# Performance work log

Hardware: AMD Instinct MI355X
Metric: run time of the kernel (lower is better)

The kernel has to match this reference:

```python
import jax, jax.numpy as jnp
import numpy as np

B, A, HR = 2, 180, 512
H_OUT = W_OUT = 512


def setup_inputs() -> dict:
    key = jax.random.key(0)
    k1, = jax.random.split(key, 1)
    sino = jax.random.normal(k1, (B, A, HR), dtype=jnp.float32)
    angles_deg = jnp.linspace(0.0, 180.0, A, endpoint=False, dtype=jnp.float32)
    return {"sino": sino, "angles_deg": angles_deg, "H": H_OUT, "W": W_OUT}


def _forward(sino, angles_deg, H, W):
    Bn, An, Hr = sino.shape
    pad = int(1.0 * 0.1 * min(H, W))  # pad_ratio = 1.0
    Hp, Wp = H + 2 * pad, W + 2 * pad

    # --- F.interpolate bilinear, align_corners=False: (A,B,Hr,1) -> (A,B,Hp,Wp).
    # Input width is 1, so width interp replicates the single column; only height interp matters.
    src = jnp.clip((jnp.arange(Hp, dtype=jnp.float32) + 0.5) * (Hr / Hp) - 0.5, 0.0, Hr - 1)
    i0 = jnp.floor(src).astype(jnp.int32)
    i1 = jnp.minimum(i0 + 1, Hr - 1)
    wH = src - i0.astype(jnp.float32)
    p = jnp.transpose(sino, (1, 0, 2)).astype(jnp.float32)  # (A,B,Hr)
    col = p[:, :, i0] * (1.0 - wH) + p[:, :, i1] * wH       # (A,B,Hp)
    proj = jnp.broadcast_to(col[:, :, :, None], (An, Bn, Hp, Wp))  # (A,B,Hp,Wp)

    # --- affine_grid (align_corners=False), sign = -1
    th = -jnp.deg2rad(angles_deg)
    c, s = jnp.cos(th), jnp.sin(th)                          # (A,)
    xs = (jnp.arange(Wp, dtype=jnp.float32) + 0.5) * (2.0 / Wp) - 1.0
    ys = (jnp.arange(Hp, dtype=jnp.float32) + 0.5) * (2.0 / Hp) - 1.0
    gx = c[:, None, None] * xs[None, None, :] - s[:, None, None] * ys[None, :, None]  # (A,Hp,Wp)
    gy = s[:, None, None] * xs[None, None, :] + c[:, None, None] * ys[None, :, None]

    # --- grid_sample bilinear, zeros padding, align_corners=False
    ix = ((gx + 1.0) * Wp - 1.0) * 0.5
    iy = ((gy + 1.0) * Hp - 1.0) * 0.5
    x0 = jnp.floor(ix).astype(jnp.int32); x1 = x0 + 1
    y0 = jnp.floor(iy).astype(jnp.int32); y1 = y0 + 1
    wx = ix - x0.astype(jnp.float32)
    wy = iy - y0.astype(jnp.float32)

    def corner(img, xi, yi, w):  # img (B,Hp,Wp); idx/w (Hp,Wp)
        valid = (xi >= 0) & (xi <= Wp - 1) & (yi >= 0) & (yi <= Hp - 1)
        xc = jnp.clip(xi, 0, Wp - 1)
        yc = jnp.clip(yi, 0, Hp - 1)
        return img[:, yc, xc] * (w * valid.astype(jnp.float32))[None]

    def sample(img, x0a, x1a, y0a, y1a, wxa, wya):
        return (corner(img, x0a, y0a, (1 - wxa) * (1 - wya)) +
                corner(img, x1a, y0a, wxa * (1 - wya)) +
                corner(img, x0a, y1a, (1 - wxa) * wya) +
                corner(img, x1a, y1a, wxa * wya))

    xr = jax.vmap(sample)(proj, x0, x1, y0, y1, wx, wy)      # (A,B,Hp,Wp)
    acc = xr.sum(axis=0) / (An + 1e-06)                      # (B,Hp,Wp)
    acc = acc[:, None, :, :]                                 # (B,1,Hp,Wp)
    if pad > 0:
        acc = acc[:, :, pad:Hp - pad, pad:Wp - pad]
    return acc


def reference(sino, angles_deg, H, W):
    return _forward(sino, angles_deg, H, W)
```

## Files before the change

### kernel.cpp

```cpp
#include <hip/hip_runtime.h>
#include <hip/hip_fp16.h>
#include <math.h>

#define B_N   2
#define A_N   180
#define HR_N  512
#define H_OUT 512
#define W_OUT 512
#define PAD   51
#define HP    614
#define WP    614
#define GUARD 80
#define HPP   (HP + 2*GUARD)
#define NPIX  (H_OUT * W_OUT)

#define TW     16
#define TH     8
#define HALF_A 90
#define CH     30
#define NCH    (HALF_A / CH)
#define WIN    20


__device__ __forceinline__ float col_val(const float* __restrict__ sino,
                                         int b, int a, int yy) {
    if (yy < 0 || yy >= HP) return 0.0f;
    float src = ((float)yy + 0.5f) * ((float)HR_N / (float)HP) - 0.5f;
    src = fminf(fmaxf(src, 0.0f), (float)(HR_N - 1));
    int i0 = (int)floorf(src);
    int i1 = min(i0 + 1, HR_N - 1);
    float wH = src - (float)i0;
    const float* srow = sino + ((size_t)b * A_N + a) * HR_N;
    return srow[i0] * (1.0f - wH) + srow[i1] * wH;
}

__global__ void prep_kernel(const float* __restrict__ sino,
                            const float* __restrict__ angles,
                            uint2* __restrict__ pk2,
                            float2* __restrict__ tg) {
    int idx = blockIdx.x * blockDim.x + threadIdx.x;
    if (idx < A_N) {
        float th = -angles[idx] * (float)(M_PI / 180.0);
        tg[idx] = make_float2(cosf(th), sinf(th));
    }
    const int total = A_N * HPP;
    if (idx < total) {
        int y = idx % HPP;
        int a = idx / HPP;
        int yy = y - GUARD;
        float v00 = col_val(sino, 0, a, yy);
        float v10 = col_val(sino, 1, a, yy);
        float v01 = col_val(sino, 0, a, yy + 1);
        float v11 = col_val(sino, 1, a, yy + 1);
        __half2 lo = __floats2half2_rn(v00, v10);
        __half2 hi = __floats2half2_rn(v01, v11);
        uint2 u;
        u.x = *(unsigned int*)&lo;
        u.y = *(unsigned int*)&hi;
        pk2[idx] = u;
    }
}

__global__ __launch_bounds__(256, 8) void bp_kernel(const uint2* __restrict__ pk2,
                                                    const float2* __restrict__ tgv,
                                                    float* __restrict__ out) {
    __shared__ int   s_base[A_N];
    __shared__ uint2 s_win[2 * CH * WIN];
    __shared__ float s_red[2][128];

    int t  = threadIdx.x;
    int tx = blockIdx.x, ty = blockIdx.y;
    float Xc = (float)(tx * TW) - 248.0f;
    float Yc = (float)(ty * TH) - 252.0f;

    if (t < A_N) {
        float2 cs = tgv[t];
        float iyc = fmaf(cs.y, Xc, fmaf(cs.x, Yc, 306.5f));
        s_base[t] = (int)floorf(iyc) - 9;
    }

    int half = t >> 7;
    int tt   = t & 127;
    int lx = tt & (TW - 1), ly = tt >> 4;
    float X = (float)(tx * TW + lx) - 255.5f;
    float Y = (float)(ty * TH + ly) - 255.5f;

    float acc0 = 0.0f, acc1 = 0.0f;
    __syncthreads();

    bool interior = (Xc * Xc + Yc * Yc) <= 87500.0f;

    for (int ch = 0; ch < NCH; ++ch) {
        for (int e = t; e < 2 * CH * WIN; e += 256) {
            int hh = e / (CH * WIN);
            int r  = e - hh * (CH * WIN);
            int la = r / WIN;
            int j  = r - la * WIN;
            int a  = hh * HALF_A + ch * CH + la;
            s_win[e] = pk2[(size_t)a * HPP + (GUARD + s_base[a] + j)];
        }
        __syncthreads();

        const int aoff = half * HALF_A + ch * CH;
        const int woff = half * (CH * WIN);
        if (interior) {
            __half2 hacc = __float2half2_rn(0.0f);
#pragma unroll
            for (int la = 0; la < CH; ++la) {
                float2 cs = tgv[aoff + la];
                float c = cs.x, s = cs.y;
                float iyc = fmaf(s, Xc, fmaf(c, Yc, 306.5f));
                float Kf  = 315.5f - floorf(iyc);
                float f   = fmaf(s, X, fmaf(c, Y, Kf));
                int   li  = (int)f;
                float wy  = f - (float)li;
                uint2 cv  = s_win[woff + la * WIN + li];
                __half2 lo = *(__half2*)&cv.x;
                __half2 hi = *(__half2*)&cv.y;
                __half2 r2 = __hfma2(__float2half2_rn(wy), __hsub2(hi, lo), lo);
                hacc = __hadd2(hacc, r2);
            }
            acc0 += __low2float(hacc);
            acc1 += __high2float(hacc);
        } else {
#pragma unroll
            for (int la = 0; la < CH; ++la) {
                float2 cs = tgv[aoff + la];
                float c = cs.x, s = cs.y;
                float iyc = fmaf(s, Xc, fmaf(c, Yc, 306.5f));
                float Kf  = 315.5f - floorf(iyc);
                float f   = fmaf(s, X, fmaf(c, Y, Kf));
                int   li  = (int)f;
                float wy  = f - (float)li;
                uint2 cv  = s_win[woff + la * WIN + li];
                __half2 lo = *(__half2*)&cv.x;
                __half2 hi = *(__half2*)&cv.y;
                __half2 r2 = __hfma2(__float2half2_rn(wy), __hsub2(hi, lo), lo);
                float ix = fmaf(c, X, fmaf(-s, Y, 306.5f));
                float xf = fminf(fmaxf(ix + 1.0f, 0.0f), 1.0f)
                         * fminf(fmaxf((float)WP - ix, 0.0f), 1.0f);
                acc0 = fmaf(xf, __low2float(r2), acc0);
                acc1 = fmaf(xf, __high2float(r2), acc1);
            }
        }
        __syncthreads();
    }

    if (half) {
        s_red[0][tt] = acc0;
        s_red[1][tt] = acc1;
    }
    __syncthreads();
    if (!half) {
        const float inv = 1.0f / (180.0f + 1e-6f);
        float a0 = (acc0 + s_red[0][tt]) * inv;
        float a1 = (acc1 + s_red[1][tt]) * inv;
        int idx = (ty * TH + ly) * W_OUT + (tx * TW + lx);
        out[idx]        = a0;
        out[NPIX + idx] = a1;
    }
}

extern "C" void kernel_launch(void* const* d_in, const int* in_sizes, int n_in,
                              void* d_out, int out_size, void* d_ws, size_t ws_size,
                              hipStream_t stream) {
    const float* sino   = (const float*)d_in[0];
    const float* angles = (const float*)d_in[1];
    char*   ws  = (char*)d_ws;
    uint2*  pk2 = (uint2*)ws;
    float2* tg  = (float2*)(ws + (size_t)A_N * HPP * sizeof(uint2));

    const int total = A_N * HPP;
    prep_kernel<<<(total + 255) / 256, 256, 0, stream>>>(sino, angles, pk2, tg);

    dim3 grid(W_OUT / TW, H_OUT / TH);
    bp_kernel<<<grid, 256, 0, stream>>>(pk2, tg, (float*)d_out);
}
```

Measured before the change: 86.66 us.

## Split angles four ways with two pixels per thread and cached trig in LDS

```diff
diff --git a/kernel.cpp b/kernel.cpp
--- a/kernel.cpp
+++ b/kernel.cpp
@@ -14,12 +14,12 @@
 #define HPP   (HP + 2*GUARD)
 #define NPIX  (H_OUT * W_OUT)
 
-#define TW     16
-#define TH     8
-#define HALF_A 90
-#define CH     30
-#define NCH    (HALF_A / CH)
-#define WIN    20
+#define TW    16
+#define TH    8
+#define QA    45
+#define CH_Q  15
+#define NCH   3
+#define WIN   20
 
 
 __device__ __forceinline__ float col_val(const float* __restrict__ sino,
@@ -61,12 +61,89 @@
     }
 }
 
+template <bool INTERIOR>
+__device__ __forceinline__ void bp_body(const uint2* __restrict__ pk2,
+                                        const float2* __restrict__ s_tg,
+                                        const int* __restrict__ s_base,
+                                        uint2* __restrict__ s_win,
+                                        int t, int q, float X, float Y,
+                                        float Xc, float Yc,
+                                        float& a00, float& a01, float& a10, float& a11) {
+    for (int ch = 0; ch < NCH; ++ch) {
+        for (int e = t; e < 4 * CH_Q * WIN; e += 256) {
+            int wid = e / WIN;
+            int j   = e - wid * WIN;
+            int qq  = wid / CH_Q;
+            int la  = wid - qq * CH_Q;
+            int a   = qq * QA + ch * CH_Q + la;
+            s_win[e] = pk2[(size_t)a * HPP + (GUARD + s_base[a] + j)];
+        }
+        __syncthreads();
+
+        const int abase = q * QA + ch * CH_Q;
+        const int wbase = q * (CH_Q * WIN);
+        if (INTERIOR) {
+            __half2 h0 = __float2half2_rn(0.0f);
+            __half2 h1 = __float2half2_rn(0.0f);
+#pragma unroll
+            for (int la = 0; la < CH_Q; ++la) {
+                float2 cs = s_tg[abase + la];
+                float c = cs.x, s = cs.y;
+                float iyc = fmaf(s, Xc, fmaf(c, Yc, 306.5f));
+                float Kf  = 315.5f - floorf(iyc);
+                float f0  = fmaf(s, X, fmaf(c, Y, Kf));
+                float f1  = f0 + s;
+                int   li0 = (int)f0;  float wy0 = f0 - (float)li0;
+                int   li1 = (int)f1;  float wy1 = f1 - (float)li1;
+                uint2 cv0 = s_win[wbase + la * WIN + li0];
+                uint2 cv1 = s_win[wbase + la * WIN + li1];
+                __half2 lo0 = *(__half2*)&cv0.x, hi0 = *(__half2*)&cv0.y;
+                __half2 lo1 = *(__half2*)&cv1.x, hi1 = *(__half2*)&cv1.y;
+                h0 = __hadd2(h0, __hfma2(__float2half2_rn(wy0), __hsub2(hi0, lo0), lo0));
+                h1 = __hadd2(h1, __hfma2(__float2half2_rn(wy1), __hsub2(hi1, lo1), lo1));
+            }
+            a00 += __low2float(h0);  a01 += __high2float(h0);
+            a10 += __low2float(h1);  a11 += __high2float(h1);
+        } else {
+#pragma unroll
+            for (int la = 0; la < CH_Q; ++la) {
+                float2 cs = s_tg[abase + la];
+                float c = cs.x, s = cs.y;
+                float iyc = fmaf(s, Xc, fmaf(c, Yc, 306.5f));
+                float Kf  = 315.5f - floorf(iyc);
+                float f0  = fmaf(s, X, fmaf(c, Y, Kf));
+                float f1  = f0 + s;
+                int   li0 = (int)f0;  float wy0 = f0 - (float)li0;
+                int   li1 = (int)f1;  float wy1 = f1 - (float)li1;
+                uint2 cv0 = s_win[wbase + la * WIN + li0];
+                uint2 cv1 = s_win[wbase + la * WIN + li1];
+                __half2 lo0 = *(__half2*)&cv0.x, hi0 = *(__half2*)&cv0.y;
+                __half2 lo1 = *(__half2*)&cv1.x, hi1 = *(__half2*)&cv1.y;
+                __half2 r0 = __hfma2(__float2half2_rn(wy0), __hsub2(hi0, lo0), lo0);
+                __half2 r1 = __hfma2(__float2half2_rn(wy1), __hsub2(hi1, lo1), lo1);
+                float ix0 = fmaf(c, X, fmaf(-s, Y, 306.5f));
+                float ix1 = ix0 + c;
+                float xf0 = fminf(fmaxf(ix0 + 1.0f, 0.0f), 1.0f)
+                          * fminf(fmaxf((float)WP - ix0, 0.0f), 1.0f);
+                float xf1 = fminf(fmaxf(ix1 + 1.0f, 0.0f), 1.0f)
+                          * fminf(fmaxf((float)WP - ix1, 0.0f), 1.0f);
+                a00 = fmaf(xf0, __low2float(r0),  a00);
+                a01 = fmaf(xf0, __high2float(r0), a01);
+                a10 = fmaf(xf1, __low2float(r1),  a10);
+                a11 = fmaf(xf1, __high2float(r1), a11);
+            }
+        }
+        __syncthreads();
+    }
+}
+
 __global__ __launch_bounds__(256, 8) void bp_kernel(const uint2* __restrict__ pk2,
                                                     const float2* __restrict__ tgv,
                                                     float* __restrict__ out) {
-    __shared__ int   s_base[A_N];
-    __shared__ uint2 s_win[2 * CH * WIN];
-    __shared__ float s_red[2][128];
+    __shared__ float2 s_tg[A_N];
+    __shared__ int    s_base[A_N];
+    __shared__ uint2  s_win[4 * CH_Q * WIN];
+    __shared__ float  s_red[3][256];
 
     int t  = threadIdx.x;
     int tx = blockIdx.x, ty = blockIdx.y;
@@ -75,89 +152,46 @@
 
     if (t < A_N) {
         float2 cs = tgv[t];
+        s_tg[t] = cs;
         float iyc = fmaf(cs.y, Xc, fmaf(cs.x, Yc, 306.5f));
         s_base[t] = (int)floorf(iyc) - 9;
     }
 
-    int half = t >> 7;
-    int tt   = t & 127;
-    int lx = tt & (TW - 1), ly = tt >> 4;
+    int q  = t >> 6;
+    int tt = t & 63;
+    int lx = (tt & 7) << 1;
+    int ly = tt >> 3;
     float X = (float)(tx * TW + lx) - 255.5f;
     float Y = (float)(ty * TH + ly) - 255.5f;
 
-    float acc0 = 0.0f, acc1 = 0.0f;
+    float a00 = 0.0f, a01 = 0.0f, a10 = 0.0f, a11 = 0.0f;
     __syncthreads();
 
     bool interior = (Xc * Xc + Yc * Yc) <= 87500.0f;
-
-    for (int ch = 0; ch < NCH; ++ch) {
-        for (int e = t; e < 2 * CH * WIN; e += 256) {
-            int hh = e / (CH * WIN);
-            int r  = e - hh * (CH * WIN);
-            int la = r / WIN;
-            int j  = r - la * WIN;
-            int a  = hh * HALF_A + ch * CH + la;
-            s_win[e] = pk2[(size_t)a * HPP + (GUARD + s_base[a] + j)];
-        }
-        __syncthreads();
-
-        const int aoff = half * HALF_A + ch * CH;
-        const int woff = half * (CH * WIN);
-        if (interior) {
-            __half2 hacc = __float2half2_rn(0.0f);
-#pragma unroll
-            for (int la = 0; la < CH; ++la) {
-                float2 cs = tgv[aoff + la];
-                float c = cs.x, s = cs.y;
-                float iyc = fmaf(s, Xc, fmaf(c, Yc, 306.5f));
-                float Kf  = 315.5f - floorf(iyc);
-                float f   = fmaf(s, X, fmaf(c, Y, Kf));
-                int   li  = (int)f;
-                float wy  = f - (float)li;
-                uint2 cv  = s_win[woff + la * WIN + li];
-                __half2 lo = *(__half2*)&cv.x;
-                __half2 hi = *(__half2*)&cv.y;
-                __half2 r2 = __hfma2(__float2half2_rn(wy), __hsub2(hi, lo), lo);
-                hacc = __hadd2(hacc, r2);
-            }
-            acc0 += __low2float(hacc);
-            acc1 += __high2float(hacc);
-        } else {
-#pragma unroll
-            for (int la = 0; la < CH; ++la) {
-                float2 cs = tgv[aoff + la];
-                float c = cs.x, s = cs.y;
-                float iyc = fmaf(s, Xc, fmaf(c, Yc, 306.5f));
-                float Kf  = 315.5f - floorf(iyc);
-                float f   = fmaf(s, X, fmaf(c, Y, Kf));
-                int   li  = (int)f;
-                float wy  = f - (float)li;
-                uint2 cv  = s_win[woff + la * WIN + li];
-                __half2 lo = *(__half2*)&cv.x;
-                __half2 hi = *(__half2*)&cv.y;
-                __half2 r2 = __hfma2(__float2half2_rn(wy), __hsub2(hi, lo), lo);
-                float ix = fmaf(c, X, fmaf(-s, Y, 306.5f));
-                float xf = fminf(fmaxf(ix + 1.0f, 0.0f), 1.0f)
-                         * fminf(fmaxf((float)WP - ix, 0.0f), 1.0f);
-                acc0 = fmaf(xf, __low2float(r2), acc0);
-                acc1 = fmaf(xf, __high2float(r2), acc1);
-            }
-        }
-        __syncthreads();
-    }
-
-    if (half) {
-        s_red[0][tt] = acc0;
-        s_red[1][tt] = acc1;
+    if (interior)
+        bp_body<true >(pk2, s_tg, s_base, s_win, t, q, X, Y, Xc, Yc, a00, a01, a10, a11);
+    else
+        bp_body<false>(pk2, s_tg, s_base, s_win, t, q, X, Y, Xc, Yc, a00, a01, a10, a11);
+
+    int pix = ly * TW + lx;
+    if (q != 0) {
+        s_red[q - 1][pix]           = a00;
+        s_red[q - 1][pix + 1]       = a10;
+        s_red[q - 1][128 + pix]     = a01;
+        s_red[q - 1][128 + pix + 1] = a11;
     }
     __syncthreads();
-    if (!half) {
+    if (q == 0) {
         const float inv = 1.0f / (180.0f + 1e-6f);
-        float a0 = (acc0 + s_red[0][tt]) * inv;
-        float a1 = (acc1 + s_red[1][tt]) * inv;
+        float r00 = (a00 + s_red[0][pix]       + s_red[1][pix]       + s_red[2][pix])       * inv;
+        float r10 = (a10 + s_red[0][pix+1]     + s_red[1][pix+1]     + s_red[2][pix+1])     * inv;
+        float r01 = (a01 + s_red[0][128+pix]   + s_red[1][128+pix]   + s_red[2][128+pix])   * inv;
+        float r11 = (a11 + s_red[0][128+pix+1] + s_red[1][128+pix+1] + s_red[2][128+pix+1]) * inv;
         int idx = (ty * TH + ly) * W_OUT + (tx * TW + lx);
-        out[idx]        = a0;
-        out[NPIX + idx] = a1;
+        out[idx]            = r00;
+        out[idx + 1]        = r10;
+        out[NPIX + idx]     = r01;
+        out[NPIX + idx + 1] = r11;
     }
 }
 
```

Result: faster. 84.09 us (-3.0%).
